# Optimization experiments

Measured on AMD Instinct MI355X. Metric: run time of the kernel, lower is better.

## Reference

```python
import jax, jax.numpy as jnp
import numpy as np

THETA = 10000.0

def apply_rope(x, token_positions, theta=THETA):
    # x: (..., seq, d_k); token_positions: (seq,)
    d_k = x.shape[-1]
    freqs = 1.0 / theta ** (jnp.arange(0, d_k, 2, dtype=jnp.float32) / d_k)  # (d_k/2,)
    ang = token_positions.astype(jnp.float32)[:, None] * freqs  # (seq, d_k/2)
    cos, sin = jnp.cos(ang), jnp.sin(ang)
    x_even, x_odd = x[..., 0::2], x[..., 1::2]
    out_even = x_even * cos - x_odd * sin
    out_odd = x_even * sin + x_odd * cos
    out = jnp.stack([out_even, out_odd], axis=-1)  # interleave pairs
    return out.reshape(*x.shape[:-1], d_k)


def setup_inputs() -> dict:
    key = jax.random.key(0)
    ks = jax.random.split(key, 5)
    B, S, D = 1, 4096, 1024
    s = 1.0 / np.sqrt(D)
    return {
        "x": jax.random.normal(ks[0], (B, S, D), dtype=jnp.float32),
        "token_positions": jnp.arange(S, dtype=jnp.int64 if jax.config.jax_enable_x64 else jnp.int32),
        "Wq": jax.random.normal(ks[1], (D, D), dtype=jnp.float32) * s,
        "Wk": jax.random.normal(ks[2], (D, D), dtype=jnp.float32) * s,
        "Wv": jax.random.normal(ks[3], (D, D), dtype=jnp.float32) * s,
        "Wo": jax.random.normal(ks[4], (D, D), dtype=jnp.float32) * s,
    }


def reference(x, token_positions, Wq, Wk, Wv, Wo):
    B, S, D = x.shape
    H = 16
    hd = D // H
    # nn.Linear(bias=False): y = x @ W.T
    q = (x @ Wq.T).reshape(B, S, H, hd).transpose(0, 2, 1, 3)  # (B,H,S,hd)
    k = (x @ Wk.T).reshape(B, S, H, hd).transpose(0, 2, 1, 3)
    v = (x @ Wv.T).reshape(B, S, H, hd).transpose(0, 2, 1, 3)
    q = apply_rope(q, token_positions)
    k = apply_rope(k, token_positions)
    scores = jnp.einsum("bhqd,bhkd->bhqk", q, k) / jnp.sqrt(jnp.float32(hd))
    causal = jnp.triu(jnp.ones((S, S), dtype=bool), k=1)  # True above diagonal
    scores = jnp.where(causal[None, None], -jnp.inf, scores)
    attn = jax.nn.softmax(scores, axis=-1)
    out = jnp.einsum("bhqk,bhkd->bhqd", attn, v)  # (B,H,S,hd)
    out = out.transpose(0, 2, 1, 3).reshape(B, S, D)
    return out @ Wo.T
```

## Files before the change

kernel.cpp:

```cpp
#include <hip/hip_runtime.h>
#include <hip/hip_bf16.h>
#include <math.h>

#define S_LEN 4096
#define D_MODEL 1024
#define NHEAD 16
#define HD 64

typedef short bf16x8 __attribute__((ext_vector_type(8)));
typedef float f32x16 __attribute__((ext_vector_type(16)));
typedef _Float16 f16x8 __attribute__((ext_vector_type(8)));
typedef _Float16 f16x4 __attribute__((ext_vector_type(4)));

static __device__ __forceinline__ unsigned pk2(float lo, float hi) {
  __hip_bfloat162 h = __float22bfloat162_rn(make_float2(lo, hi));
  return *reinterpret_cast<unsigned*>(&h);
}

static __device__ __forceinline__ void gload16(const void* g, void* l) {
  __builtin_amdgcn_global_load_lds(
      (const __attribute__((address_space(1))) unsigned*)g,
      (__attribute__((address_space(3))) unsigned*)l, 16, 0, 0);
}

__global__ __launch_bounds__(256)
void cvt_f16(const float* __restrict__ src, _Float16* __restrict__ dst, int n4) {
  for (int i = blockIdx.x * 256 + threadIdx.x; i < n4; i += gridDim.x * 256) {
    float4 v = ((const float4*)src)[i];
    f16x4 o;
    o[0] = (_Float16)v.x; o[1] = (_Float16)v.y;
    o[2] = (_Float16)v.z; o[3] = (_Float16)v.w;
    ((f16x4*)dst)[i] = o;
  }
}

__global__ __launch_bounds__(256)
void cvt4_f16(const float* __restrict__ s0, const float* __restrict__ s1,
              const float* __restrict__ s2, const float* __restrict__ s3,
              _Float16* __restrict__ d0, _Float16* __restrict__ d1,
              _Float16* __restrict__ d2, _Float16* __restrict__ d3, int n4) {
  const float* s = (blockIdx.y == 0) ? s0 : (blockIdx.y == 1) ? s1
                 : (blockIdx.y == 2) ? s2 : s3;
  _Float16* d = (blockIdx.y == 0) ? d0 : (blockIdx.y == 1) ? d1
              : (blockIdx.y == 2) ? d2 : d3;
  for (int i = blockIdx.x * 256 + threadIdx.x; i < n4; i += gridDim.x * 256) {
    float4 v = ((const float4*)s)[i];
    f16x4 o;
    o[0] = (_Float16)v.x; o[1] = (_Float16)v.y;
    o[2] = (_Float16)v.z; o[3] = (_Float16)v.w;
    ((f16x4*)d)[i] = o;
  }
}

__global__ __launch_bounds__(256)
void vtrans(const unsigned short* __restrict__ V, unsigned short* __restrict__ Vt) {
  __shared__ unsigned short t[64][72];
  const int tid = threadIdx.x;
  const int k0 = blockIdx.x * 64;
  const int n0 = blockIdx.y * 64;
#pragma unroll
  for (int p = 0; p < 2; ++p) {
    int idx = tid + p * 256;
    int r = idx >> 3, c8 = idx & 7;
    *(bf16x8*)&t[r][c8 * 8] =
        *(const bf16x8*)(V + (size_t)(k0 + r) * D_MODEL + n0 + c8 * 8);
  }
  __syncthreads();
  const int d = tid >> 2, kc = tid & 3;
  __align__(16) unsigned short buf[16];
#pragma unroll
  for (int j = 0; j < 16; ++j) buf[j] = t[kc * 16 + j][d];
  *(uint4*)(Vt + (size_t)(n0 + d) * S_LEN + k0 + kc * 16) = *(uint4*)buf;
  *(uint4*)(Vt + (size_t)(n0 + d) * S_LEN + k0 + kc * 16 + 8) = *(uint4*)(buf + 8);
}

#define BUFBYTES 16384

static __device__ __forceinline__ void gemm_mainloop_f16(
    const _Float16* __restrict__ A, const _Float16* __restrict__ B,
    int tr0, int br0, char* ldsbuf, int tid,
    f32x16& acc00, f32x16& acc01, f32x16& acc10, f32x16& acc11) {
  const int lane = tid & 63, w = tid >> 6;
  const int l31 = lane & 31, hi5 = lane >> 5;
  const int wr = (w >> 1) * 64, wc = (w & 1) * 64;

  const _Float16* srcs[4];
  int offs[4];
#pragma unroll
  for (int j = 0; j < 4; ++j) {
    int ch = w + 4 * j;
    if (ch < 8) {
      int u = ch * 64 + lane;
      srcs[j] = A + (size_t)(tr0 + (u & 127)) * 1024 + (u >> 7) * 8;
      offs[j] = ch * 1024;
    } else {
      int u = (ch - 8) * 64 + lane;
      srcs[j] = B + (size_t)(br0 + (u & 127)) * 1024 + (u >> 7) * 8;
      offs[j] = 8192 + (ch - 8) * 1024;
    }
  }

#define STAGE(bufoff, koff)                                           \
  {                                                                   \
    _Pragma("unroll") for (int j = 0; j < 4; ++j)                     \
        gload16(srcs[j] + (koff), ldsbuf + (bufoff) + offs[j]);       \
  }

#define COMPUTE(bufoff)                                               \
  {                                                                   \
    const char* lb = ldsbuf + (bufoff);                               \
    _Pragma("unroll") for (int s = 0; s < 2; ++s) {                   \
      const int c = 2 * s + hi5;                                      \
      const char* pa = lb + (size_t)(c * 128 + wr + l31) * 16;        \
      f16x8 a0 = *(const f16x8*)(pa);                                 \
      f16x8 a1 = *(const f16x8*)(pa + 512);                           \
      const char* pb = lb + 8192 + (size_t)(c * 128 + wc + l31) * 16; \
      f16x8 b0 = *(const f16x8*)(pb);                                 \
      f16x8 b1 = *(const f16x8*)(pb + 512);                           \
      acc00 = __builtin_amdgcn_mfma_f32_32x32x16_f16(a0, b0, acc00, 0, 0, 0); \
      acc01 = __builtin_amdgcn_mfma_f32_32x32x16_f16(a0, b1, acc01, 0, 0, 0); \
      acc10 = __builtin_amdgcn_mfma_f32_32x32x16_f16(a1, b0, acc10, 0, 0, 0); \
      acc11 = __builtin_amdgcn_mfma_f32_32x32x16_f16(a1, b1, acc11, 0, 0, 0); \
    }                                                                 \
  }

  STAGE(0, 0);
  __syncthreads();

#pragma unroll 1
  for (int it = 0; it < 16; ++it) {
    const int t0 = 2 * it;
    if (t0 < 31) STAGE(BUFBYTES, (t0 + 1) * 32);
    COMPUTE(0);
    __syncthreads();
    if (t0 + 1 < 31) STAGE(0, (t0 + 2) * 32);
    COMPUTE(BUFBYTES);
    __syncthreads();
  }
#undef STAGE
#undef COMPUTE
}

__global__ __launch_bounds__(256)
void qkv_gemm(const _Float16* __restrict__ xf,
              const _Float16* __restrict__ wqf, const _Float16* __restrict__ wkf,
              const _Float16* __restrict__ wvf,
              unsigned short* __restrict__ Qo, unsigned short* __restrict__ Ko,
              unsigned short* __restrict__ Vo, const int* __restrict__ pos) {
  __shared__ __align__(16) char ldsbuf[2 * BUFBYTES];
  const int tid = threadIdx.x;
  const int nb = blockIdx.x;
  const int which = nb >> 3;
  const int br0 = (nb & 7) * 128;
  const int tr0 = blockIdx.y * 128;

  const _Float16* Bsrc = (which == 0) ? wqf : (which == 1) ? wkf : wvf;
  unsigned short* Out = (which == 0) ? Qo : (which == 1) ? Ko : Vo;

  f32x16 acc00, acc01, acc10, acc11;
#pragma unroll
  for (int r = 0; r < 16; ++r) {
    acc00[r] = 0.0f; acc01[r] = 0.0f; acc10[r] = 0.0f; acc11[r] = 0.0f;
  }

  gemm_mainloop_f16(xf, Bsrc, tr0, br0, ldsbuf, tid, acc00, acc01, acc10, acc11);

  const int lane = tid & 63, w = tid >> 6;
  const int l31 = lane & 31, hi5 = lane >> 5;
  const int wr = (w >> 1) * 64, wc = (w & 1) * 64;
  const float qs = (which == 0) ? 0.125f * 1.44269504088896f : 1.0f;

#pragma unroll
  for (int bc = 0; bc < 2; ++bc) {
    const int n = br0 + wc + bc * 32 + l31;
    const int ch = n & 63;
    const float fr = 1.0f / powf(10000.0f, (float)(ch & ~1) * (1.0f / 64.0f));
#pragma unroll
    for (int ar = 0; ar < 2; ++ar) {
      const f32x16& a = ar ? (bc ? acc11 : acc10) : (bc ? acc01 : acc00);
#pragma unroll
      for (int r = 0; r < 16; ++r) {
        const int m = tr0 + wr + ar * 32 + (r & 3) + 8 * (r >> 2) + 4 * hi5;
        float v = a[r];
        if (which < 2) {
          const float ang = (float)pos[m] * fr;
          float sn, cs;
          __sincosf(ang, &sn, &cs);
          const float vp = __shfl_xor(v, 1);
          v = (ch & 1) ? (vp * sn + v * cs) : (v * cs - vp * sn);
          v *= qs;
        }
        const float nv = __shfl_xor(v, 1);
        if ((ch & 1) == 0) {
          *(unsigned*)(Out + (size_t)m * 1024 + n) = pk2(v, nv);
        }
      }
    }
  }
}

__global__ __launch_bounds__(256)
void out_gemm(const _Float16* __restrict__ Of, const _Float16* __restrict__ Wof,
              float* __restrict__ out) {
  __shared__ __align__(16) char ldsbuf[2 * BUFBYTES];
  const int tid = threadIdx.x;
  const int br0 = blockIdx.x * 128;
  const int tr0 = blockIdx.y * 128;

  f32x16 acc00, acc01, acc10, acc11;
#pragma unroll
  for (int r = 0; r < 16; ++r) {
    acc00[r] = 0.0f; acc01[r] = 0.0f; acc10[r] = 0.0f; acc11[r] = 0.0f;
  }

  gemm_mainloop_f16(Of, Wof, tr0, br0, ldsbuf, tid, acc00, acc01, acc10, acc11);

  const int lane = tid & 63, w = tid >> 6;
  const int l31 = lane & 31, hi5 = lane >> 5;
  const int wr = (w >> 1) * 64, wc = (w & 1) * 64;
#pragma unroll
  for (int bc = 0; bc < 2; ++bc) {
    const int n = br0 + wc + bc * 32 + l31;
#pragma unroll
    for (int ar = 0; ar < 2; ++ar) {
      const f32x16& a = ar ? (bc ? acc11 : acc10) : (bc ? acc01 : acc00);
#pragma unroll
      for (int r = 0; r < 16; ++r) {
        const int m = tr0 + wr + ar * 32 + (r & 3) + 8 * (r >> 2) + 4 * hi5;
        out[(size_t)m * 1024 + n] = a[r];
      }
    }
  }
}

union __align__(16) AttnSmem {
  unsigned short q[128 * 64];
  struct { unsigned short k[64 * 64]; unsigned short vt[64 * 64]; } kv;
  float oep[4][32][68];
};

__global__ __launch_bounds__(256)
void attn_mfma(const unsigned short* __restrict__ Qg, const unsigned short* __restrict__ Kg,
               const unsigned short* __restrict__ Vt, _Float16* __restrict__ Of) {
  __shared__ AttnSmem sm;
  const int tid = threadIdx.x;
  const int lane = tid & 63;
  const int w = tid >> 6;
  const int h = blockIdx.x & 15;
  const int qb = 31 - (blockIdx.x >> 4);
  const int qrow0 = qb * 128;
  const int l31 = lane & 31;
  const int hi = lane >> 5;

  {
    const unsigned short* src = Qg + (size_t)qrow0 * D_MODEL + h * HD;
#pragma unroll
    for (int p = 0; p < 4; ++p) {
      int idx = tid + p * 256;
      int row = idx >> 3, c8 = idx & 7;
      bf16x8 v = *(const bf16x8*)(src + (size_t)row * D_MODEL + c8 * 8);
      *(bf16x8*)((char*)sm.q + row * 128 + ((c8 * 16) ^ ((row & 7) << 4))) = v;
    }
  }
  __syncthreads();

  bf16x8 qf[4];
  {
    int qr = w * 32 + l31;
    char* rb = (char*)sm.q + qr * 128;
    int sw = (qr & 7) << 4;
#pragma unroll
    for (int s = 0; s < 4; ++s)
      qf[s] = *(const bf16x8*)(rb + ((s * 32 + hi * 16) ^ sw));
  }
  __syncthreads();

  f32x16 oacc0, oacc1;
#pragma unroll
  for (int r = 0; r < 16; ++r) { oacc0[r] = 0.0f; oacc1[r] = 0.0f; }
  float m_ = -1e30f, l_ = 0.0f;
  const int qg = qrow0 + w * 32 + l31;
  const int qwmax = qrow0 + w * 32 + 31;
  const int nT = 2 * qb + 2;

  const int sr0 = tid >> 3, sc0 = tid & 7;
  const int sr1 = sr0 + 32;
  const int swz = (sc0 * 16) ^ ((sr0 & 7) << 4);
  const unsigned short* srcK = Kg + h * HD;
  const unsigned short* srcVt = Vt + (size_t)(h * HD) * S_LEN;

  bf16x8 kA0, kA1, vA0, vA1, kB0, kB1, vB0, vB1;

#define LOADKV(K0, K1, V0, V1, t)                                        \
  if ((t) < nT) {                                                        \
    const int kk = (t) * 64;                                             \
    K0 = *(const bf16x8*)(srcK + (size_t)(kk + sr0) * D_MODEL + sc0 * 8);\
    K1 = *(const bf16x8*)(srcK + (size_t)(kk + sr1) * D_MODEL + sc0 * 8);\
    V0 = *(const bf16x8*)(srcVt + (size_t)sr0 * S_LEN + kk + sc0 * 8);   \
    V1 = *(const bf16x8*)(srcVt + (size_t)sr1 * S_LEN + kk + sc0 * 8);   \
  }

#define WRITEKV(K0, K1, V0, V1)                                          \
  {                                                                      \
    *(bf16x8*)((char*)sm.kv.k + sr0 * 128 + swz) = K0;                   \
    *(bf16x8*)((char*)sm.kv.k + sr1 * 128 + swz) = K1;                   \
    *(bf16x8*)((char*)sm.kv.vt + sr0 * 128 + swz) = V0;                  \
    *(bf16x8*)((char*)sm.kv.vt + sr1 * 128 + swz) = V1;                  \
  }

#define COMPUTE_TILE(t)                                                  \
  {                                                                      \
    const int k0 = (t) * 64;                                             \
    _Pragma("unroll") for (int kh = 0; kh < 2; ++kh) {                   \
      if (k0 + kh * 32 > qwmax) continue;                                \
      f32x16 sa;                                                         \
      _Pragma("unroll") for (int r = 0; r < 16; ++r) sa[r] = 0.0f;       \
      {                                                                  \
        int krow = kh * 32 + l31;                                        \
        char* kb = (char*)sm.kv.k + krow * 128;                          \
        int sw = (krow & 7) << 4;                                        \
        __builtin_amdgcn_s_setprio(1);                                   \
        _Pragma("unroll") for (int s = 0; s < 4; ++s) {                  \
          bf16x8 kf = *(const bf16x8*)(kb + ((s * 32 + hi * 16) ^ sw));  \
          sa = __builtin_amdgcn_mfma_f32_32x32x16_bf16(kf, qf[s], sa, 0, 0, 0); \
        }                                                                \
        __builtin_amdgcn_s_setprio(0);                                   \
      }                                                                  \
      if (k0 + kh * 32 + 31 > qg) {                                      \
        _Pragma("unroll") for (int r = 0; r < 16; ++r) {                 \
          int kg = k0 + kh * 32 + (r & 3) + 8 * (r >> 2) + 4 * hi;       \
          if (kg > qg) sa[r] = -1e30f;                                   \
        }                                                                \
      }                                                                  \
                                      \
      float x0 = fmaxf(fmaxf(sa[0], sa[1]), sa[2]);                      \
      float x1 = fmaxf(fmaxf(sa[3], sa[4]), sa[5]);                      \
      float x2 = fmaxf(fmaxf(sa[6], sa[7]), sa[8]);                      \
      float x3 = fmaxf(fmaxf(sa[9], sa[10]), sa[11]);                    \
      float x4 = fmaxf(fmaxf(sa[12], sa[13]), sa[14]);                   \
      float tm = fmaxf(fmaxf(x0, x1), x2);                               \
      tm = fmaxf(fmaxf(tm, x3), x4);                                     \
      tm = fmaxf(tm, sa[15]);                                            \
      tm = fmaxf(tm, __shfl_xor(tm, 32));                                \
      if (!__all(tm <= m_ + 8.0f)) {                                     \
        const float mn = fmaxf(m_, tm);                                  \
        const float sc = exp2f(m_ - mn);                                 \
        m_ = mn;                                                         \
        l_ *= sc;                                                        \
        _Pragma("unroll") for (int r = 0; r < 16; ++r) {                 \
          oacc0[r] *= sc; oacc1[r] *= sc;                                \
        }                                                                \
      }                                                                  \
      float rs = 0.0f;                                                   \
      _Pragma("unroll") for (int r = 0; r < 16; ++r) {                   \
        float e = exp2f(sa[r] - m_);                                     \
        sa[r] = e;                                                       \
        rs += e;                                                         \
      }                                                                  \
      rs += __shfl_xor(rs, 32);                                          \
      l_ += rs;                                                          \
      unsigned a0 = pk2(sa[0], sa[1]),  b0 = pk2(sa[4], sa[5]);          \
      unsigned a1 = pk2(sa[2], sa[3]),  b1 = pk2(sa[6], sa[7]);          \
      unsigned a2 = pk2(sa[8], sa[9]),  b2 = pk2(sa[12], sa[13]);        \
      unsigned a3 = pk2(sa[10], sa[11]), b3 = pk2(sa[14], sa[15]);       \
      asm volatile("v_permlane32_swap_b32 %0, %1" : "+v"(a0), "+v"(b0)); \
      asm volatile("v_permlane32_swap_b32 %0, %1" : "+v"(a1), "+v"(b1)); \
      asm volatile("v_permlane32_swap_b32 %0, %1" : "+v"(a2), "+v"(b2)); \
      asm volatile("v_permlane32_swap_b32 %0, %1" : "+v"(a3), "+v"(b3)); \
      union FU { unsigned u[4]; bf16x8 v; } f0, f1;                      \
      f0.u[0] = a0; f0.u[1] = a1; f0.u[2] = b0; f0.u[3] = b1;            \
      f1.u[0] = a2; f1.u[1] = a3; f1.u[2] = b2; f1.u[3] = b3;            \
      {                                                                  \
        char* vb0 = (char*)sm.kv.vt + l31 * 128;                         \
        char* vb1 = (char*)sm.kv.vt + (32 + l31) * 128;                  \
        int sw = (l31 & 7) << 4;                                         \
        int off0 = (kh * 64 + hi * 16) ^ sw;                             \
        int off1 = (kh * 64 + 32 + hi * 16) ^ sw;                        \
        bf16x8 v00 = *(const bf16x8*)(vb0 + off0);                       \
        bf16x8 v01 = *(const bf16x8*)(vb0 + off1);                       \
        bf16x8 v10 = *(const bf16x8*)(vb1 + off0);                       \
        bf16x8 v11 = *(const bf16x8*)(vb1 + off1);                       \
        __builtin_amdgcn_s_setprio(1);                                   \
        oacc0 = __builtin_amdgcn_mfma_f32_32x32x16_bf16(v00, f0.v, oacc0, 0, 0, 0); \
        oacc0 = __builtin_amdgcn_mfma_f32_32x32x16_bf16(v01, f1.v, oacc0, 0, 0, 0); \
        oacc1 = __builtin_amdgcn_mfma_f32_32x32x16_bf16(v10, f0.v, oacc1, 0, 0, 0); \
        oacc1 = __builtin_amdgcn_mfma_f32_32x32x16_bf16(v11, f1.v, oacc1, 0, 0, 0); \
        __builtin_amdgcn_s_setprio(0);                                   \
      }                                                                  \
    }                                                                    \
  }

  LOADKV(kA0, kA1, vA0, vA1, 0);

#pragma unroll 1
  for (int tt = 0; tt < nT; tt += 2) {
    __syncthreads();
    WRITEKV(kA0, kA1, vA0, vA1);
    LOADKV(kB0, kB1, vB0, vB1, tt + 1);
    __syncthreads();
    COMPUTE_TILE(tt);
    __syncthreads();
    WRITEKV(kB0, kB1, vB0, vB1);
    LOADKV(kA0, kA1, vA0, vA1, tt + 2);
    __syncthreads();
    COMPUTE_TILE(tt + 1);
  }
#undef LOADKV
#undef WRITEKV
#undef COMPUTE_TILE

  __syncthreads();
  const float inv = 1.0f / l_;
#pragma unroll
  for (int g = 0; g < 4; ++g) {
    *(float4*)&sm.oep[w][l31][8 * g + 4 * hi] =
        make_float4(oacc0[4*g+0] * inv, oacc0[4*g+1] * inv,
                    oacc0[4*g+2] * inv, oacc0[4*g+3] * inv);
    *(float4*)&sm.oep[w][l31][8 * g + 4 * hi + 32] =
        make_float4(oacc1[4*g+0] * inv, oacc1[4*g+1] * inv,
                    oacc1[4*g+2] * inv, oacc1[4*g+3] * inv);
  }
  {
    int qr = lane >> 1, chh = lane & 1;
    const float* rp = &sm.oep[w][qr][chh * 32];
    const size_t base = (size_t)(qrow0 + w * 32 + qr) * D_MODEL + h * HD + chh * 32;
#pragma unroll
    for (int j = 0; j < 8; ++j) {
      float4 v = *(const float4*)(rp + j * 4);
      f16x4 o;
      o[0] = (_Float16)v.x; o[1] = (_Float16)v.y;
      o[2] = (_Float16)v.z; o[3] = (_Float16)v.w;
      *(f16x4*)(Of + base + j * 4) = o;
    }
  }
}

extern "C" void kernel_launch(void* const* d_in, const int* in_sizes, int n_in,
                              void* d_out, int out_size, void* d_ws, size_t ws_size,
                              hipStream_t stream) {
  const float* x   = (const float*)d_in[0];
  const int*   pos = (const int*)d_in[1];
  const float* Wq  = (const float*)d_in[2];
  const float* Wk  = (const float*)d_in[3];
  const float* Wv  = (const float*)d_in[4];
  const float* Wo  = (const float*)d_in[5];
  float* out = (float*)d_out;

  char* ws = (char*)d_ws;
  const size_t MB = 1024 * 1024;
  _Float16* xf  = (_Float16*)(ws);
  _Float16* wqf = (_Float16*)(ws + 8 * MB);
  _Float16* wkf = (_Float16*)(ws + 10 * MB);
  _Float16* wvf = (_Float16*)(ws + 12 * MB);
  _Float16* wof = (_Float16*)(ws + 14 * MB);
  unsigned short* Qb = (unsigned short*)(ws + 16 * MB);
  unsigned short* Kb = (unsigned short*)(ws + 24 * MB);
  unsigned short* Vb = (unsigned short*)(ws + 32 * MB);
  unsigned short* Vt = (unsigned short*)(ws + 40 * MB);
  _Float16* Of = xf;

  dim3 blk(256);

  hipLaunchKernelGGL(cvt_f16, dim3(2048), blk, 0, stream, x, xf,
                     (int)((size_t)S_LEN * D_MODEL / 4));
  hipLaunchKernelGGL(cvt4_f16, dim3(512, 4), blk, 0, stream,
                     Wq, Wk, Wv, Wo, wqf, wkf, wvf, wof,
                     D_MODEL * D_MODEL / 4);

  hipLaunchKernelGGL(qkv_gemm, dim3(24, 32), blk, 0, stream,
                     xf, wqf, wkf, wvf, Qb, Kb, Vb, pos);

  hipLaunchKernelGGL(vtrans, dim3(64, 16), blk, 0, stream, Vb, Vt);

  hipLaunchKernelGGL(attn_mfma, dim3(512), blk, 0, stream, Qb, Kb, Vt, Of);

  hipLaunchKernelGGL(out_gemm, dim3(8, 32), blk, 0, stream, Of, wof, out);
}
```

Baseline: 326.7 us.

## Double-buffer attention K/V tiles via direct global-to-LDS loads with smaller blocks

Reworks the attention kernel to use 128-thread blocks covering 64 query rows each, doubling the grid to 1024 blocks. K and V^T tiles are now fetched straight into a double-buffered LDS region with global_load_lds. The XOR swizzle is applied on the source address, so no register staging or separate LDS stores are needed. The loop overlaps the next tile's load with the current tile's compute and uses one barrier per tile instead of four. The costs are a larger LDS footprint for the two buffers and a reliance on the compiler inserting the correct vmcnt waits before each barrier.

```diff
diff --git a/kernel.cpp b/kernel.cpp
--- a/kernel.cpp
+++ b/kernel.cpp
@@ -234,12 +234,14 @@
 }
 
 union __align__(16) AttnSmem {
-  unsigned short q[128 * 64];
-  struct { unsigned short k[64 * 64]; unsigned short vt[64 * 64]; } kv;
-  float oep[4][32][68];
+  struct {
+    unsigned short q[64 * 64];
+    unsigned short kv[2][2][64 * 64];
+  } s;
+  float oep[2][32][68];
 };
 
-__global__ __launch_bounds__(256)
+__global__ __launch_bounds__(128)
 void attn_mfma(const unsigned short* __restrict__ Qg, const unsigned short* __restrict__ Kg,
                const unsigned short* __restrict__ Vt, _Float16* __restrict__ Of) {
   __shared__ AttnSmem sm;
@@ -247,8 +249,8 @@
   const int lane = tid & 63;
   const int w = tid >> 6;
   const int h = blockIdx.x & 15;
-  const int qb = 31 - (blockIdx.x >> 4);
-  const int qrow0 = qb * 128;
+  const int qb = 63 - (blockIdx.x >> 4);
+  const int qrow0 = qb * 64;
   const int l31 = lane & 31;
   const int hi = lane >> 5;
 
@@ -256,10 +258,10 @@
     const unsigned short* src = Qg + (size_t)qrow0 * D_MODEL + h * HD;
 #pragma unroll
     for (int p = 0; p < 4; ++p) {
-      int idx = tid + p * 256;
+      int idx = tid + p * 128;
       int row = idx >> 3, c8 = idx & 7;
       bf16x8 v = *(const bf16x8*)(src + (size_t)row * D_MODEL + c8 * 8);
-      *(bf16x8*)((char*)sm.q + row * 128 + ((c8 * 16) ^ ((row & 7) << 4))) = v;
+      *(bf16x8*)((char*)sm.s.q + row * 128 + ((c8 * 16) ^ ((row & 7) << 4))) = v;
     }
   }
   __syncthreads();
@@ -267,13 +269,12 @@
   bf16x8 qf[4];
   {
     int qr = w * 32 + l31;
-    char* rb = (char*)sm.q + qr * 128;
+    char* rb = (char*)sm.s.q + qr * 128;
     int sw = (qr & 7) << 4;
 #pragma unroll
     for (int s = 0; s < 4; ++s)
       qf[s] = *(const bf16x8*)(rb + ((s * 32 + hi * 16) ^ sw));
   }
-  __syncthreads();
 
   f32x16 oacc0, oacc1;
 #pragma unroll
@@ -281,43 +282,41 @@
   float m_ = -1e30f, l_ = 0.0f;
   const int qg = qrow0 + w * 32 + l31;
   const int qwmax = qrow0 + w * 32 + 31;
-  const int nT = 2 * qb + 2;
-
-  const int sr0 = tid >> 3, sc0 = tid & 7;
-  const int sr1 = sr0 + 32;
-  const int swz = (sc0 * 16) ^ ((sr0 & 7) << 4);
-  const unsigned short* srcK = Kg + h * HD;
-  const unsigned short* srcVt = Vt + (size_t)(h * HD) * S_LEN;
-
-  bf16x8 kA0, kA1, vA0, vA1, kB0, kB1, vB0, vB1;
-
-#define LOADKV(K0, K1, V0, V1, t)                                        \
+  const int nT = qb + 1;
+
+  const int rowb = 32 * w + (lane >> 3);
+  const int chnk = (lane & 7) ^ ((lane >> 3) & 7);
+  const unsigned short* kbase = Kg + h * HD + (size_t)rowb * D_MODEL + chnk * 8;
+  const unsigned short* vbase = Vt + (size_t)(h * HD + rowb) * S_LEN + chnk * 8;
+
+#define STAGE(buf, t)                                                    \
   if ((t) < nT) {                                                        \
-    const int kk = (t) * 64;                                             \
-    K0 = *(const bf16x8*)(srcK + (size_t)(kk + sr0) * D_MODEL + sc0 * 8);\
-    K1 = *(const bf16x8*)(srcK + (size_t)(kk + sr1) * D_MODEL + sc0 * 8);\
-    V0 = *(const bf16x8*)(srcVt + (size_t)sr0 * S_LEN + kk + sc0 * 8);   \
-    V1 = *(const bf16x8*)(srcVt + (size_t)sr1 * S_LEN + kk + sc0 * 8);   \
-  }
-
-#define WRITEKV(K0, K1, V0, V1)                                          \
-  {                                                                      \
-    *(bf16x8*)((char*)sm.kv.k + sr0 * 128 + swz) = K0;                   \
-    *(bf16x8*)((char*)sm.kv.k + sr1 * 128 + swz) = K1;                   \
-    *(bf16x8*)((char*)sm.kv.vt + sr0 * 128 + swz) = V0;                  \
-    *(bf16x8*)((char*)sm.kv.vt + sr1 * 128 + swz) = V1;                  \
-  }
-
-#define COMPUTE_TILE(t)                                                  \
+    const unsigned short* kp = kbase + (size_t)(t) * 64 * D_MODEL;       \
+    const unsigned short* vp = vbase + (t) * 64;                         \
+    char* kd = (char*)sm.s.kv[buf][0] + w * 4096;                        \
+    char* vd = (char*)sm.s.kv[buf][1] + w * 4096;                        \
+    gload16(kp,                      kd);                                \
+    gload16(kp +  8 * D_MODEL,       kd + 1024);                         \
+    gload16(kp + 16 * D_MODEL,       kd + 2048);                         \
+    gload16(kp + 24 * D_MODEL,       kd + 3072);                         \
+    gload16(vp,                      vd);                                \
+    gload16(vp +  8 * S_LEN,         vd + 1024);                         \
+    gload16(vp + 16 * S_LEN,         vd + 2048);                         \
+    gload16(vp + 24 * S_LEN,         vd + 3072);                         \
+  }
+
+#define COMPUTE_TILE(buf, t)                                             \
   {                                                                      \
     const int k0 = (t) * 64;                                             \
+    char* kvk = (char*)sm.s.kv[buf][0];                                  \
+    char* kvv = (char*)sm.s.kv[buf][1];                                  \
     _Pragma("unroll") for (int kh = 0; kh < 2; ++kh) {                   \
       if (k0 + kh * 32 > qwmax) continue;                                \
       f32x16 sa;                                                         \
       _Pragma("unroll") for (int r = 0; r < 16; ++r) sa[r] = 0.0f;       \
       {                                                                  \
         int krow = kh * 32 + l31;                                        \
-        char* kb = (char*)sm.kv.k + krow * 128;                          \
+        char* kb = kvk + krow * 128;                                     \
         int sw = (krow & 7) << 4;                                        \
         __builtin_amdgcn_s_setprio(1);                                   \
         _Pragma("unroll") for (int s = 0; s < 4; ++s) {                  \
@@ -371,8 +370,8 @@
       f0.u[0] = a0; f0.u[1] = a1; f0.u[2] = b0; f0.u[3] = b1;            \
       f1.u[0] = a2; f1.u[1] = a3; f1.u[2] = b2; f1.u[3] = b3;            \
       {                                                                  \
-        char* vb0 = (char*)sm.kv.vt + l31 * 128;                         \
-        char* vb1 = (char*)sm.kv.vt + (32 + l31) * 128;                  \
+        char* vb0 = kvv + l31 * 128;                                     \
+        char* vb1 = kvv + (32 + l31) * 128;                              \
         int sw = (l31 & 7) << 4;                                         \
         int off0 = (kh * 64 + hi * 16) ^ sw;                             \
         int off1 = (kh * 64 + 32 + hi * 16) ^ sw;                        \
@@ -390,26 +389,18 @@
     }                                                                    \
   }
 
-  LOADKV(kA0, kA1, vA0, vA1, 0);
+  STAGE(0, 0);
+  __syncthreads();
 
 #pragma unroll 1
-  for (int tt = 0; tt < nT; tt += 2) {
+  for (int t = 0; t < nT; ++t) {
+    STAGE((t + 1) & 1, t + 1);
+    COMPUTE_TILE(t & 1, t);
     __syncthreads();
-    WRITEKV(kA0, kA1, vA0, vA1);
-    LOADKV(kB0, kB1, vB0, vB1, tt + 1);
-    __syncthreads();
-    COMPUTE_TILE(tt);
-    __syncthreads();
-    WRITEKV(kB0, kB1, vB0, vB1);
-    LOADKV(kA0, kA1, vA0, vA1, tt + 2);
-    __syncthreads();
-    COMPUTE_TILE(tt + 1);
-  }
-#undef LOADKV
-#undef WRITEKV
+  }
+#undef STAGE
 #undef COMPUTE_TILE
 
-  __syncthreads();
   const float inv = 1.0f / l_;
 #pragma unroll
   for (int g = 0; g < 4; ++g) {
@@ -472,7 +463,7 @@
 
   hipLaunchKernelGGL(vtrans, dim3(64, 16), blk, 0, stream, Vb, Vt);
 
-  hipLaunchKernelGGL(attn_mfma, dim3(512), blk, 0, stream, Qb, Kb, Vt, Of);
+  hipLaunchKernelGGL(attn_mfma, dim3(1024), dim3(128), 0, stream, Qb, Kb, Vt, Of);
 
   hipLaunchKernelGGL(out_gemm, dim3(8, 32), blk, 0, stream, Of, wof, out);
 }
```

Result: slower. 336.1 us (+2.9%).
